# Kernel tuning notes

Hardware: AMD Instinct MI355X
Metric: run time of the kernel (lower is better)

The kernel has to match this reference:

```python
import jax, jax.numpy as jnp
from jax import lax
import numpy as np

B, T, N = 64, 512, 80
HT, HV, HI = 512, 1024, 512  # textual, visual, ilstm hidden sizes


def setup_inputs() -> dict:
    key = jax.random.key(0)
    ks = jax.random.split(key, 12)
    s = 0.02
    return {
        "h_v": jax.random.normal(ks[0], (B, T, HV), jnp.float32),
        "h_s": jax.random.normal(ks[1], (B, N, HT), jnp.float32),
        "W_S": jax.random.normal(ks[2], (HI, HT), jnp.float32) * s,
        "b_S": jnp.zeros((HI,), jnp.float32),
        "W_V": jax.random.normal(ks[3], (HI, HV), jnp.float32) * s,
        "b_V": jnp.zeros((HI,), jnp.float32),
        "W_R": jax.random.normal(ks[4], (HI, HI), jnp.float32) * s,
        "b_R": jnp.zeros((HI,), jnp.float32),
        "W_w": jax.random.normal(ks[5], (1, HI), jnp.float32) * s,
        "b_w": jnp.zeros((1,), jnp.float32),
        "W_ih": jax.random.normal(ks[6], (4 * HI, HT + HV), jnp.float32) * s,
        "b_ih": jnp.zeros((4 * HI,), jnp.float32),
        "W_hh": jax.random.normal(ks[7], (4 * HI, HI), jnp.float32) * s,
        "b_hh": jnp.zeros((4 * HI,), jnp.float32),
    }


def reference(h_v, h_s, W_S, b_S, W_V, b_V, W_R, b_R, W_w, b_w, W_ih, b_ih, W_hh, b_hh):
    n_batch, T_, _ = h_v.shape
    Hi = W_R.shape[0]
    dt = h_v.dtype
    # loop-invariant textual projection, hoisted: (B, N, Hi)
    S_proj = jnp.einsum('bnt,it->bni', h_s, W_S) + b_S
    # visual projection for all timesteps: (B, T, Hi)
    V_proj = jnp.einsum('btv,iv->bti', h_v, W_V) + b_V

    def step(carry, xs):
        h_prev, c_prev = carry
        v_t, hv_t = xs  # (B, Hi), (B, Hv)
        r_proj = h_prev @ W_R.T + b_R  # (B, Hi)
        pre = jnp.tanh(S_proj + (r_proj + v_t)[:, None, :])  # (B, N, Hi)
        beta = jnp.einsum('bni,i->bn', pre, W_w[0]) + b_w[0]  # (B, N)
        # NOTE: faithful to source -- softmax over the BATCH dim (dim=0)
        alpha = jax.nn.softmax(beta, axis=0)
        H_t_s = jnp.einsum('bnt,bn->bt', h_s, alpha)  # (B, Ht)
        r_t = jnp.concatenate([hv_t, H_t_s], axis=1)  # (B, Hv+Ht)
        gates = r_t @ W_ih.T + b_ih + h_prev @ W_hh.T + b_hh  # (B, 4Hi)
        i_g, f_g, g_g, o_g = jnp.split(gates, 4, axis=1)
        c_new = jax.nn.sigmoid(f_g) * c_prev + jax.nn.sigmoid(i_g) * jnp.tanh(g_g)
        h_new = jax.nn.sigmoid(o_g) * jnp.tanh(c_new)
        return (h_new, c_new), h_new

    init = (jnp.zeros((n_batch, Hi), dt), jnp.zeros((n_batch, Hi), dt))
    xs = (jnp.swapaxes(V_proj, 0, 1), jnp.swapaxes(h_v, 0, 1))  # time-major
    _, hs = lax.scan(step, init, xs)  # (T, B, Hi)
    return jnp.swapaxes(hs, 0, 1)  # (B, T, Hi)
```

## Files before the change

kernel.cpp:

```cpp
#include <hip/hip_runtime.h>


typedef unsigned short ushort_t;
typedef unsigned int uint_t;
typedef __attribute__((ext_vector_type(8))) short bf16x8;
typedef __attribute__((ext_vector_type(4))) float f32x4;

#define MFMA_BF16 __builtin_amdgcn_mfma_f32_16x16x32_bf16

__device__ __forceinline__ float bf2f(ushort_t u) {
  return __builtin_bit_cast(float, (uint_t)u << 16);
}
__device__ __forceinline__ ushort_t f2bf(float f) {
  uint_t u = __builtin_bit_cast(uint_t, f);
  u += 0x7FFFu + ((u >> 16) & 1u);
  return (ushort_t)(u >> 16);
}
__device__ __forceinline__ uint_t pk(float lo, float hi) {
  return (uint_t)f2bf(lo) | ((uint_t)f2bf(hi) << 16);
}
__device__ __forceinline__ void stage16(ushort_t* dst, const float* src) {
  float4 a = *(const float4*)src,     b = *(const float4*)(src + 4);
  float4 c = *(const float4*)(src + 8), d = *(const float4*)(src + 12);
  uint4 lo = { pk(a.x,a.y), pk(a.z,a.w), pk(b.x,b.y), pk(b.z,b.w) };
  uint4 hi = { pk(c.x,c.y), pk(c.z,c.w), pk(d.x,d.y), pk(d.z,d.w) };
  *(uint4*)dst = lo; *(uint4*)(dst + 8) = hi;
}
__device__ __forceinline__ bf16x8 cvt8(const float* src) {
  float4 a = *(const float4*)src, b = *(const float4*)(src + 4);
  uint4 u = { pk(a.x,a.y), pk(a.z,a.w), pk(b.x,b.y), pk(b.z,b.w) };
  return __builtin_bit_cast(bf16x8, u);
}
__device__ __forceinline__ float tanh_(float x) {
  float e = __expf(2.f * x);
  return 1.f - 2.f * __builtin_amdgcn_rcpf(e + 1.f);
}
__device__ __forceinline__ float sigm_(float x) {
  return __builtin_amdgcn_rcpf(1.f + __expf(-x));
}

__device__ __forceinline__ float ldcg_f(const float* p) {
  return __hip_atomic_load(p, __ATOMIC_RELAXED, __HIP_MEMORY_SCOPE_AGENT);
}
__device__ __forceinline__ void stcg_f(float* p, float v) {
  __hip_atomic_store(p, v, __ATOMIC_RELAXED, __HIP_MEMORY_SCOPE_AGENT);
}
__device__ __forceinline__ uint_t ldcg_u(const uint_t* p) {
  return __hip_atomic_load(p, __ATOMIC_RELAXED, __HIP_MEMORY_SCOPE_AGENT);
}
__device__ __forceinline__ void stcg_u(uint_t* p, uint_t v) {
  __hip_atomic_store(p, v, __ATOMIC_RELAXED, __HIP_MEMORY_SCOPE_AGENT);
}

__global__ __launch_bounds__(256) void cvt_kernel(
    const float* __restrict__ in, ushort_t* __restrict__ out, int n4) {
  int i = blockIdx.x * blockDim.x + threadIdx.x;
  if (i < n4) {
    float4 v = ((const float4*)in)[i];
    uint2 r = { pk(v.x, v.y), pk(v.z, v.w) };
    ((uint2*)out)[i] = r;
  }
}

__global__ __launch_bounds__(256) void pack_frag_kernel(
    const float* __restrict__ src, int ld, int coff,
    ushort_t* __restrict__ out, int mode, int lkc) {
  size_t o = ((size_t)blockIdx.x * 256 + threadIdx.x) * 8;
  int lane = (int)((o >> 3) & 63);
  int kc   = (int)((o >> 9) & ((1u << lkc) - 1u));
  int tile = (int)(o >> (9 + lkc));
  int row  = mode ? ((tile & 3) * 512 + (tile >> 2) * 16 + (lane & 15))
                  : (tile * 16 + (lane & 15));
  int col  = kc * 32 + (lane >> 4) * 8;
  const float* s = &src[(size_t)row * ld + coff + col];
  float4 a = *(const float4*)s, b = *(const float4*)(s + 4);
  uint4 u = { pk(a.x,a.y), pk(a.z,a.w), pk(b.x,b.y), pk(b.z,b.w) };
  *(uint4*)&out[o] = u;
}

__global__ __launch_bounds__(256) void gemm_bt(
    const float* __restrict__ A, int lda,
    const float* __restrict__ W, int ldw,
    const float* __restrict__ bias1,
    ushort_t* __restrict__ out, int ldo, int K, int tmaj)
{
  __shared__ __align__(16) ushort_t sA[128][32];
  __shared__ __align__(16) ushort_t sW[128][32];
  const int tid = threadIdx.x;
  const int col0 = blockIdx.x * 128, row0 = blockIdx.y * 128;
  const int lane = tid & 63, wv = tid >> 6;
  const int wr = (wv & 1) * 64, wc = (wv >> 1) * 64;
  const int fr = lane & 15, quad = lane >> 4;
  const int sr = tid >> 1, skk = (tid & 1) * 16;
  f32x4 acc[4][4] = {};
  for (int k0 = 0; k0 < K; k0 += 32) {
    stage16(&sA[sr][skk], &A[(size_t)(row0 + sr) * lda + k0 + skk]);
    stage16(&sW[sr][skk], &W[(size_t)(col0 + sr) * ldw + k0 + skk]);
    __syncthreads();
    bf16x8 af[4], wf[4];
    #pragma unroll
    for (int mt = 0; mt < 4; ++mt) af[mt] = *(const bf16x8*)&sA[wr + mt*16 + fr][quad*8];
    #pragma unroll
    for (int nt = 0; nt < 4; ++nt) wf[nt] = *(const bf16x8*)&sW[wc + nt*16 + fr][quad*8];
    #pragma unroll
    for (int mt = 0; mt < 4; ++mt)
      #pragma unroll
      for (int nt = 0; nt < 4; ++nt)
        acc[mt][nt] = MFMA_BF16(af[mt], wf[nt], acc[mt][nt], 0, 0, 0);
    __syncthreads();
  }
  #pragma unroll
  for (int nt = 0; nt < 4; ++nt) {
    int col = col0 + wc + nt*16 + fr;
    float bs = bias1 ? bias1[col] : 0.f;
    #pragma unroll
    for (int mt = 0; mt < 4; ++mt)
      #pragma unroll
      for (int r = 0; r < 4; ++r) {
        int row = row0 + wr + mt*16 + quad*4 + r;
        int orow = tmaj ? ((row & 511) * 64 + (row >> 9)) : row;
        out[(size_t)orow * ldo + col] = f2bf(acc[mt][nt][r] + bs);
      }
  }
}

__device__ __forceinline__ void spin_gen(unsigned* gen, unsigned g, unsigned* dead) {
  int n = 0;
  while (__hip_atomic_load(gen, __ATOMIC_RELAXED, __HIP_MEMORY_SCOPE_AGENT) == g) {
    __builtin_amdgcn_s_sleep(4);
    if (++n > 20000) {
      __hip_atomic_store(dead, 1u, __ATOMIC_RELAXED, __HIP_MEMORY_SCOPE_AGENT);
      break;
    }
    if ((n & 1023) == 0 &&
        __hip_atomic_load(dead, __ATOMIC_RELAXED, __HIP_MEMORY_SCOPE_AGENT) != 0u)
      break;
  }
}

__device__ __forceinline__ void grid_sync(unsigned* bar) {
  __syncthreads();
  if (threadIdx.x == 0) {
    unsigned* gen  = bar + 288;
    unsigned* dead = bar + 320;
    if (__hip_atomic_load(dead, __ATOMIC_RELAXED, __HIP_MEMORY_SCOPE_AGENT) == 0u) {
      unsigned g = __hip_atomic_load(gen, __ATOMIC_RELAXED, __HIP_MEMORY_SCOPE_AGENT);
      unsigned grp = blockIdx.x & 7u;
      unsigned old = __hip_atomic_fetch_add(bar + grp * 32, 1u,
                        __ATOMIC_RELAXED, __HIP_MEMORY_SCOPE_AGENT);
      if (old == 31u) {
        unsigned r = __hip_atomic_fetch_add(bar + 256, 1u,
                        __ATOMIC_RELAXED, __HIP_MEMORY_SCOPE_AGENT);
        if (r == 7u) {
          #pragma unroll
          for (int i = 0; i < 8; ++i)
            __hip_atomic_store(bar + i * 32, 0u, __ATOMIC_RELAXED, __HIP_MEMORY_SCOPE_AGENT);
          __hip_atomic_store(bar + 256, 0u, __ATOMIC_RELAXED, __HIP_MEMORY_SCOPE_AGENT);
          __builtin_amdgcn_s_waitcnt(0);
          __hip_atomic_store(gen, g + 1u, __ATOMIC_RELAXED, __HIP_MEMORY_SCOPE_AGENT);
        } else {
          spin_gen(gen, g, dead);
        }
      } else {
        spin_gen(gen, g, dead);
      }
    }
  }
  __syncthreads();
}

struct LoopArgs {
  const ushort_t *Sproj, *Vproj, *Xproj;
  const ushort_t *WRf, *Whhf, *Wqf, *Wihf;
  const ushort_t *hsb;
  const float *bR, *Ww, *bih, *bhh, *hv;
  float *ru, *expb, *s4;
  uint_t *hrep, *hsrep;
  unsigned *bar;
  float *out;
};


__global__ __launch_bounds__(512, 2) void loop_kernel(LoopArgs p) {
  const int blk = blockIdx.x, tid = threadIdx.x;
  const int lane = tid & 63, wv = tid >> 6;
  const int fr = lane & 15, quad = lane >> 4;
  const int b4 = (blk & 7) * 8 + (blk >> 5);
  const int q4 = (blk >> 3) & 3;

  const bool isGate = (blk < 128);
  const bool isRu   = (blk >= 128) && (blk < 144);
  const int mtG = blk >> 5;
  const int jt  = (blk & 7) * 4 + ((blk >> 3) & 3);
  const int g   = wv & 3, kh = wv >> 2;
  const int mtR = (blk - 128) >> 2;
  const int ct  = ((blk - 128) & 3) * 8 + wv;

  __shared__ __align__(16) uint_t sH[4096];
  __shared__ __align__(16) float s_ru[512];
  __shared__ __align__(16) float s_ww[512];
  __shared__ __align__(16) float s_red[512];
  __shared__ __align__(16) float s_acc[8][256];
  __shared__ float s_hsv[128];
  __shared__ float s_alpha[80];
  __shared__ float s_hh[256];
  __shared__ float s_bias[64];

  s_ww[tid] = p.Ww[tid];
  if (isGate && tid < 64) {
    int n = (tid >> 4) * 512 + jt * 16 + (tid & 15);
    s_bias[tid] = p.bih[n] + p.bhh[n];
  }
  float c_reg = 0.f;

  bf16x8 wf2[16];
  bf16x8 wfx[16];
  if (isGate) {
    #pragma unroll
    for (int kc = 0; kc < 8; ++kc) {
      int kcg = kh * 8 + kc;
      wf2[kc]     = *(const bf16x8*)&p.Whhf[((size_t)(jt*4+g)*16 + kcg)*512 + lane*8];
      wf2[8 + kc] = *(const bf16x8*)&p.Wqf [((size_t)(jt*4+g)*16 + kcg)*512 + lane*8];
    }
    if (!p.Xproj) {
      #pragma unroll
      for (int kc = 0; kc < 16; ++kc)
        wfx[kc] = *(const bf16x8*)&p.Wihf[((size_t)(jt*4+g)*32 + kh*16 + kc)*512 + lane*8];
    }
  } else if (isRu) {
    #pragma unroll
    for (int kc = 0; kc < 16; ++kc)
      wf2[kc] = *(const bf16x8*)&p.WRf[((size_t)ct*16 + kc)*512 + lane*8];
  }
  __syncthreads();

  f32x4 accA = {};
  for (int t = 0; t < 512; ++t) {
    if (isGate) {
      f32x4 acc = {};
      if (!p.Xproj) {
        int row = mtG * 16 + fr;
        #pragma unroll
        for (int kc = 0; kc < 16; ++kc) {
          bf16x8 af = cvt8(&p.hv[((size_t)row * 512 + t) * 1024 + kh*512 + kc*32 + quad*8]);
          acc = MFMA_BF16(af, wfx[kc], acc, 0, 0, 0);
        }
      }
      if (t) {
        const uint_t* src = p.hrep + mtG * 4096;
        uint_t hst[8];
        #pragma unroll
        for (int i = 0; i < 8; ++i) hst[i] = ldcg_u(src + i * 512 + tid);
        #pragma unroll
        for (int i = 0; i < 8; ++i) sH[i * 512 + tid] = hst[i];
        __syncthreads();
        #pragma unroll
        for (int kc = 0; kc < 8; ++kc) {
          int kcg = kh * 8 + kc;
          bf16x8 af = *(const bf16x8*)&sH[kcg * 256 + quad * 64 + fr * 4];
          acc = MFMA_BF16(af, wf2[kc], acc, 0, 0, 0);
        }
      }
      accA = acc;
    } else if (isRu) {
      f32x4 acc = {};
      if (t) {
        const uint_t* src = p.hrep + mtR * 4096;
        uint_t hst[8];
        #pragma unroll
        for (int i = 0; i < 8; ++i) hst[i] = ldcg_u(src + i * 512 + tid);
        #pragma unroll
        for (int i = 0; i < 8; ++i) sH[i * 512 + tid] = hst[i];
        __syncthreads();
        #pragma unroll
        for (int kc = 0; kc < 16; ++kc) {
          bf16x8 af = *(const bf16x8*)&sH[kc * 256 + quad * 64 + fr * 4];
          acc = MFMA_BF16(af, wf2[kc], acc, 0, 0, 0);
        }
      }
      #pragma unroll
      for (int r = 0; r < 4; ++r) {
        int row = mtR * 16 + quad * 4 + r, col = ct * 16 + fr;
        float v = acc[r] + p.bR[col] + bf2f(p.Vproj[(size_t)t * 32768 + row * 512 + col]);
        stcg_f(&p.ru[row * 512 + col], v);
      }
    }
    grid_sync(p.bar);

    s_ru[tid] = ldcg_f(&p.ru[b4 * 512 + tid]);
    __syncthreads();
    #pragma unroll
    for (int rr = 0; rr < 3; ++rr) {
      int nl = wv + 8 * rr;
      if (nl < 20) {
        int n = q4 * 20 + nl;
        uint4 sv = *(const uint4*)&p.Sproj[((size_t)(b4 * 80 + n)) * 512 + lane * 8];
        float4 r0 = *(const float4*)&s_ru[lane * 8];
        float4 r1 = *(const float4*)&s_ru[lane * 8 + 4];
        float4 w0 = *(const float4*)&s_ww[lane * 8];
        float4 w1 = *(const float4*)&s_ww[lane * 8 + 4];
        float a = 0.f;
        a += tanh_(bf2f((ushort_t)(sv.x & 0xFFFF)) + r0.x) * w0.x;
        a += tanh_(bf2f((ushort_t)(sv.x >> 16))    + r0.y) * w0.y;
        a += tanh_(bf2f((ushort_t)(sv.y & 0xFFFF)) + r0.z) * w0.z;
        a += tanh_(bf2f((ushort_t)(sv.y >> 16))    + r0.w) * w0.w;
        a += tanh_(bf2f((ushort_t)(sv.z & 0xFFFF)) + r1.x) * w1.x;
        a += tanh_(bf2f((ushort_t)(sv.z >> 16))    + r1.y) * w1.y;
        a += tanh_(bf2f((ushort_t)(sv.w & 0xFFFF)) + r1.z) * w1.z;
        a += tanh_(bf2f((ushort_t)(sv.w >> 16))    + r1.w) * w1.w;
        #pragma unroll
        for (int off = 32; off > 0; off >>= 1) a += __shfl_xor(a, off, 64);
        if (lane == 0) {
          float e = __expf(a);
          stcg_f(&p.expb[b4 * 80 + n], e);
          __hip_atomic_fetch_add(&p.s4[(t & 1) * 320 + (b4 & 3) * 80 + n], e,
                                 __ATOMIC_RELAXED, __HIP_MEMORY_SCOPE_AGENT);
        }
      }
    }
    grid_sync(p.bar);

    if (tid < 80) {
      const float* sc = p.s4 + (t & 1) * 320;
      float s = ldcg_f(sc + tid) + ldcg_f(sc + 80 + tid) +
                ldcg_f(sc + 160 + tid) + ldcg_f(sc + 240 + tid);
      float e = ldcg_f(&p.expb[b4 * 80 + tid]);
      s_alpha[tid] = e * __builtin_amdgcn_rcpf(s);
    }
    if (blk == 0 && tid < 320)
      stcg_f(&p.s4[((t + 1) & 1) * 320 + tid], 0.f);
    __syncthreads();
    {
      int nq = tid >> 7, jl = tid & 127;
      const ushort_t* hp = p.hsb + (size_t)b4 * 40960 + q4 * 128 + jl;
      float part = 0.f;
      #pragma unroll 5
      for (int n0 = 0; n0 < 20; ++n0) {
        int n = nq * 20 + n0;
        part += s_alpha[n] * bf2f(hp[(size_t)n * 512]);
      }
      s_red[tid] = part;
    }
    __syncthreads();
    if (tid < 128)
      s_hsv[tid] = s_red[tid] + s_red[128 + tid] + s_red[256 + tid] + s_red[384 + tid];
    __syncthreads();
    if (tid < 64) {
      int c = q4 * 128 + tid * 2;
      int kc = c >> 5, qd = (c >> 3) & 3, e2 = (c & 7) >> 1;
      int dw = (((b4 >> 4) * 16 + kc) * 4 + qd) * 64 + (b4 & 15) * 4 + e2;
      stcg_u(&p.hsrep[dw], pk(s_hsv[tid * 2], s_hsv[tid * 2 + 1]));
    }
    grid_sync(p.bar);

    if (isGate) {
      const uint_t* src = p.hsrep + mtG * 4096;
      uint_t hst[8];
      #pragma unroll
      for (int i = 0; i < 8; ++i) hst[i] = ldcg_u(src + i * 512 + tid);
      #pragma unroll
      for (int i = 0; i < 8; ++i) sH[i * 512 + tid] = hst[i];
      __syncthreads();
      f32x4 acc = accA;
      #pragma unroll
      for (int kc = 0; kc < 8; ++kc) {
        int kcg = kh * 8 + kc;
        bf16x8 af = *(const bf16x8*)&sH[kcg * 256 + quad * 64 + fr * 4];
        acc = MFMA_BF16(af, wf2[8 + kc], acc, 0, 0, 0);
      }
      #pragma unroll
      for (int r = 0; r < 4; ++r) s_acc[wv][(quad * 4 + r) * 16 + fr] = acc[r];
      __syncthreads();
      if (tid < 256) {
        int b = tid >> 4, jj = tid & 15, bi = tid;
        float g0 = s_acc[0][bi] + s_acc[4][bi] + s_bias[jj];
        float g1 = s_acc[1][bi] + s_acc[5][bi] + s_bias[16 + jj];
        float g2 = s_acc[2][bi] + s_acc[6][bi] + s_bias[32 + jj];
        float g3 = s_acc[3][bi] + s_acc[7][bi] + s_bias[48 + jj];
        if (p.Xproj) {
          const ushort_t* xp = &p.Xproj[(size_t)t * 131072 +
                                        (size_t)(mtG * 16 + b) * 2048 + jt * 16 + jj];
          g0 += bf2f(xp[0]);    g1 += bf2f(xp[512]);
          g2 += bf2f(xp[1024]); g3 += bf2f(xp[1536]);
        }
        float ig = sigm_(g0), fg = sigm_(g1), gv = tanh_(g2), og = sigm_(g3);
        float cn = fg * c_reg + ig * gv;
        c_reg = cn;
        float hn = og * tanh_(cn);
        s_hh[bi] = hn;
        p.out[((size_t)(mtG * 16 + b) * 512 + t) * 512 + jt * 16 + jj] = hn;
      }
      __syncthreads();
      if (tid < 128) {
        int b = tid >> 3, jp = tid & 7;
        int c = jt * 16 + jp * 2;
        int kc = c >> 5, qd = (c >> 3) & 3, e2 = (c & 7) >> 1;
        int dw = ((mtG * 16 + kc) * 4 + qd) * 64 + b * 4 + e2;
        stcg_u(&p.hrep[dw], pk(s_hh[b * 16 + jp * 2], s_hh[b * 16 + jp * 2 + 1]));
      }
    }
    grid_sync(p.bar);
  }
}

extern "C" void kernel_launch(void* const* d_in, const int* in_sizes, int n_in,
                              void* d_out, int out_size, void* d_ws, size_t ws_size,
                              hipStream_t stream) {
  (void)in_sizes; (void)n_in; (void)out_size;
  const float* hv   = (const float*)d_in[0];
  const float* hs   = (const float*)d_in[1];
  const float* W_S  = (const float*)d_in[2];
  const float* b_S  = (const float*)d_in[3];
  const float* W_V  = (const float*)d_in[4];
  const float* b_V  = (const float*)d_in[5];
  const float* W_R  = (const float*)d_in[6];
  const float* b_R  = (const float*)d_in[7];
  const float* W_w  = (const float*)d_in[8];
  const float* W_ih = (const float*)d_in[10];
  const float* b_ih = (const float*)d_in[11];
  const float* W_hh = (const float*)d_in[12];
  const float* b_hh = (const float*)d_in[13];

  char* ws = (char*)d_ws;
  unsigned long long off = 0;
  auto alloc = [&](unsigned long long bytes) {
    unsigned long long pp = off; off += (bytes + 255ull) & ~255ull; return pp;
  };
  ushort_t* Sproj = (ushort_t*)(ws + alloc(5120ull * 512 * 2));
  ushort_t* Vproj = (ushort_t*)(ws + alloc(512ull * 64 * 512 * 2));
  ushort_t* hsb   = (ushort_t*)(ws + alloc(64ull * 80 * 512 * 2));
  ushort_t* WRf   = (ushort_t*)(ws + alloc(512ull * 512 * 2));
  ushort_t* Whhf  = (ushort_t*)(ws + alloc(2048ull * 512 * 2));
  ushort_t* Wqf   = (ushort_t*)(ws + alloc(2048ull * 512 * 2));
  float*    ru    = (float*)(ws + alloc(64ull * 512 * 4));
  float*    expb  = (float*)(ws + alloc(64ull * 80 * 4));
  unsigned long long zoff = off;
  uint_t*   hrep  = (uint_t*)(ws + alloc(16384ull * 4));
  uint_t*   hsrep = (uint_t*)(ws + alloc(16384ull * 4));
  float*    s4    = (float*)(ws + alloc(2ull * 4 * 80 * 4));
  unsigned* bar   = (unsigned*)(ws + alloc(2048));
  unsigned long long zsize = off - zoff;
  unsigned long long tail = off;
  bool precX = ws_size >= tail + 512ull * 64 * 2048 * 2 + 4096;
  ushort_t* Xproj = precX ? (ushort_t*)(ws + tail) : nullptr;
  ushort_t* Wihf  = precX ? nullptr : (ushort_t*)(ws + tail);

  cvt_kernel<<<2560, 256, 0, stream>>>(hs, hsb, 64 * 80 * 512 / 4);
  pack_frag_kernel<<<128, 256, 0, stream>>>(W_R,  512,  0,    WRf,  0, 4);
  pack_frag_kernel<<<512, 256, 0, stream>>>(W_hh, 512,  0,    Whhf, 1, 4);
  pack_frag_kernel<<<512, 256, 0, stream>>>(W_ih, 1536, 1024, Wqf,  1, 4);
  if (!precX)
    pack_frag_kernel<<<1024, 256, 0, stream>>>(W_ih, 1536, 0, Wihf, 1, 5);

  gemm_bt<<<dim3(4, 40), 256, 0, stream>>>(hs, 512, W_S, 512, b_S, Sproj, 512, 512, 0);
  gemm_bt<<<dim3(4, 256), 256, 0, stream>>>(hv, 1024, W_V, 1024, b_V, Vproj, 512, 1024, 1);
  if (precX)
    gemm_bt<<<dim3(16, 256), 256, 0, stream>>>(hv, 1024, W_ih, 1536, nullptr, Xproj, 2048, 1024, 1);

  hipMemsetAsync(ws + zoff, 0, (size_t)zsize, stream);

  LoopArgs la;
  la.Sproj = Sproj; la.Vproj = Vproj; la.Xproj = Xproj;
  la.WRf = WRf; la.Whhf = Whhf; la.Wqf = Wqf; la.Wihf = Wihf;
  la.hsb = hsb;
  la.bR = b_R; la.Ww = W_w; la.bih = b_ih; la.bhh = b_hh; la.hv = hv;
  la.ru = ru; la.expb = expb; la.s4 = s4;
  la.hrep = hrep; la.hsrep = hsrep; la.bar = bar; la.out = (float*)d_out;
  loop_kernel<<<256, 512, 0, stream>>>(la);
}
```

Measured before the change: 12.41 ms.

## Partition persistent grid into batch groups with local barriers and counter handoff

```diff
diff --git a/kernel.cpp b/kernel.cpp
--- a/kernel.cpp
+++ b/kernel.cpp
@@ -138,24 +138,23 @@
   }
 }
 
-__device__ __forceinline__ void grid_sync(unsigned* bar) {
+__device__ __forceinline__ void sync_bar(unsigned* base, unsigned sub,
+                                         unsigned sub_last, unsigned* dead) {
   __syncthreads();
   if (threadIdx.x == 0) {
-    unsigned* gen  = bar + 288;
-    unsigned* dead = bar + 320;
+    unsigned* gen = base + 288;
     if (__hip_atomic_load(dead, __ATOMIC_RELAXED, __HIP_MEMORY_SCOPE_AGENT) == 0u) {
       unsigned g = __hip_atomic_load(gen, __ATOMIC_RELAXED, __HIP_MEMORY_SCOPE_AGENT);
-      unsigned grp = blockIdx.x & 7u;
-      unsigned old = __hip_atomic_fetch_add(bar + grp * 32, 1u,
+      unsigned old = __hip_atomic_fetch_add(base + sub * 32, 1u,
                         __ATOMIC_RELAXED, __HIP_MEMORY_SCOPE_AGENT);
-      if (old == 31u) {
-        unsigned r = __hip_atomic_fetch_add(bar + 256, 1u,
+      if (old == sub_last) {
+        unsigned r = __hip_atomic_fetch_add(base + 256, 1u,
                         __ATOMIC_RELAXED, __HIP_MEMORY_SCOPE_AGENT);
         if (r == 7u) {
           #pragma unroll
           for (int i = 0; i < 8; ++i)
-            __hip_atomic_store(bar + i * 32, 0u, __ATOMIC_RELAXED, __HIP_MEMORY_SCOPE_AGENT);
-          __hip_atomic_store(bar + 256, 0u, __ATOMIC_RELAXED, __HIP_MEMORY_SCOPE_AGENT);
+            __hip_atomic_store(base + i * 32, 0u, __ATOMIC_RELAXED, __HIP_MEMORY_SCOPE_AGENT);
+          __hip_atomic_store(base + 256, 0u, __ATOMIC_RELAXED, __HIP_MEMORY_SCOPE_AGENT);
           __builtin_amdgcn_s_waitcnt(0);
           __hip_atomic_store(gen, g + 1u, __ATOMIC_RELAXED, __HIP_MEMORY_SCOPE_AGENT);
         } else {
@@ -185,16 +184,17 @@
   const int blk = blockIdx.x, tid = threadIdx.x;
   const int lane = tid & 63, wv = tid >> 6;
   const int fr = lane & 15, quad = lane >> 4;
-  const int b4 = (blk & 7) * 8 + (blk >> 5);
-  const int q4 = (blk >> 3) & 3;
-
-  const bool isGate = (blk < 128);
-  const bool isRu   = (blk >= 128) && (blk < 144);
-  const int mtG = blk >> 5;
-  const int jt  = (blk & 7) * 4 + ((blk >> 3) & 3);
-  const int g   = wv & 3, kh = wv >> 2;
-  const int mtR = (blk - 128) >> 2;
-  const int ct  = ((blk - 128) & 3) * 8 + wv;
+  const int G = blk >> 6, w6 = blk & 63;
+  const int b4 = G * 16 + (w6 & 15), q = w6 >> 4;
+  const bool isGate = (w6 < 32);
+  const bool isRu   = (w6 >= 32) && (w6 < 36);
+  const int jt = w6 & 31;
+  const int g = wv & 3, kh = wv >> 2;
+  const int ct = ((w6 - 32) & 3) * 8 + wv;
+
+  unsigned* dead = p.bar + 320;
+  unsigned* rcnt = p.bar + 384 + G;
+  unsigned* gbar = p.bar + 512 + G * 512;
 
   __shared__ __align__(16) uint_t sH[4096];
   __shared__ __align__(16) float s_ru[512];
@@ -236,10 +236,11 @@
 
   f32x4 accA = {};
   for (int t = 0; t < 512; ++t) {
+    float x0 = 0.f, x1 = 0.f, x2 = 0.f, x3 = 0.f;
     if (isGate) {
       f32x4 acc = {};
       if (!p.Xproj) {
-        int row = mtG * 16 + fr;
+        int row = G * 16 + fr;
         #pragma unroll
         for (int kc = 0; kc < 16; ++kc) {
           bf16x8 af = cvt8(&p.hv[((size_t)row * 512 + t) * 1024 + kh*512 + kc*32 + quad*8]);
@@ -247,7 +248,7 @@
         }
       }
       if (t) {
-        const uint_t* src = p.hrep + mtG * 4096;
+        const uint_t* src = p.hrep + G * 4096;
         uint_t hst[8];
         #pragma unroll
         for (int i = 0; i < 8; ++i) hst[i] = ldcg_u(src + i * 512 + tid);
@@ -262,10 +263,16 @@
         }
       }
       accA = acc;
+      if (p.Xproj && tid < 256) {
+        const ushort_t* xp = &p.Xproj[(size_t)t * 131072 +
+                                      (size_t)(G * 16 + (tid >> 4)) * 2048 + jt * 16 + (tid & 15)];
+        x0 = bf2f(xp[0]);    x1 = bf2f(xp[512]);
+        x2 = bf2f(xp[1024]); x3 = bf2f(xp[1536]);
+      }
     } else if (isRu) {
       f32x4 acc = {};
       if (t) {
-        const uint_t* src = p.hrep + mtR * 4096;
+        const uint_t* src = p.hrep + G * 4096;
         uint_t hst[8];
         #pragma unroll
         for (int i = 0; i < 8; ++i) hst[i] = ldcg_u(src + i * 512 + tid);
@@ -280,20 +287,35 @@
       }
       #pragma unroll
       for (int r = 0; r < 4; ++r) {
-        int row = mtR * 16 + quad * 4 + r, col = ct * 16 + fr;
+        int row = G * 16 + quad * 4 + r, col = ct * 16 + fr;
         float v = acc[r] + p.bR[col] + bf2f(p.Vproj[(size_t)t * 32768 + row * 512 + col]);
         stcg_f(&p.ru[row * 512 + col], v);
       }
-    }
-    grid_sync(p.bar);
-
+      __syncthreads();
+      if (tid == 0)
+        __hip_atomic_fetch_add(rcnt, 1u, __ATOMIC_RELAXED, __HIP_MEMORY_SCOPE_AGENT);
+    }
+
+    if (tid == 0) {
+      unsigned thr = 4u * (unsigned)(t + 1);
+      int n = 0;
+      while (ldcg_u(rcnt) < thr) {
+        __builtin_amdgcn_s_sleep(4);
+        if (++n > 20000) {
+          stcg_u(dead, 1u);
+          break;
+        }
+        if ((n & 1023) == 0 && ldcg_u(dead) != 0u) break;
+      }
+    }
+    __syncthreads();
     s_ru[tid] = ldcg_f(&p.ru[b4 * 512 + tid]);
     __syncthreads();
     #pragma unroll
     for (int rr = 0; rr < 3; ++rr) {
       int nl = wv + 8 * rr;
       if (nl < 20) {
-        int n = q4 * 20 + nl;
+        int n = q * 20 + nl;
         uint4 sv = *(const uint4*)&p.Sproj[((size_t)(b4 * 80 + n)) * 512 + lane * 8];
         float4 r0 = *(const float4*)&s_ru[lane * 8];
         float4 r1 = *(const float4*)&s_ru[lane * 8 + 4];
@@ -312,27 +334,27 @@
         for (int off = 32; off > 0; off >>= 1) a += __shfl_xor(a, off, 64);
         if (lane == 0) {
           float e = __expf(a);
-          stcg_f(&p.expb[b4 * 80 + n], e);
-          __hip_atomic_fetch_add(&p.s4[(t & 1) * 320 + (b4 & 3) * 80 + n], e,
+          stcg_f(&p.expb[(t & 1) * 5120 + n * 64 + b4], e);
+          __hip_atomic_fetch_add(&p.s4[(t % 3) * 320 + G * 80 + n], e,
                                  __ATOMIC_RELAXED, __HIP_MEMORY_SCOPE_AGENT);
         }
       }
     }
-    grid_sync(p.bar);
+    sync_bar(p.bar, (unsigned)(blk & 7), 31u, dead);
 
     if (tid < 80) {
-      const float* sc = p.s4 + (t & 1) * 320;
+      const float* sc = p.s4 + (t % 3) * 320;
       float s = ldcg_f(sc + tid) + ldcg_f(sc + 80 + tid) +
                 ldcg_f(sc + 160 + tid) + ldcg_f(sc + 240 + tid);
-      float e = ldcg_f(&p.expb[b4 * 80 + tid]);
-      s_alpha[tid] = e * __builtin_amdgcn_rcpf(s);
+      float num = ldcg_f(&p.expb[(t & 1) * 5120 + tid * 64 + b4]);
+      s_alpha[tid] = num * __builtin_amdgcn_rcpf(s);
     }
     if (blk == 0 && tid < 320)
-      stcg_f(&p.s4[((t + 1) & 1) * 320 + tid], 0.f);
+      stcg_f(&p.s4[((t + 2) % 3) * 320 + tid], 0.f);
     __syncthreads();
     {
       int nq = tid >> 7, jl = tid & 127;
-      const ushort_t* hp = p.hsb + (size_t)b4 * 40960 + q4 * 128 + jl;
+      const ushort_t* hp = p.hsb + (size_t)b4 * 40960 + q * 128 + jl;
       float part = 0.f;
       #pragma unroll 5
       for (int n0 = 0; n0 < 20; ++n0) {
@@ -346,15 +368,15 @@
       s_hsv[tid] = s_red[tid] + s_red[128 + tid] + s_red[256 + tid] + s_red[384 + tid];
     __syncthreads();
     if (tid < 64) {
-      int c = q4 * 128 + tid * 2;
+      int c = q * 128 + tid * 2;
       int kc = c >> 5, qd = (c >> 3) & 3, e2 = (c & 7) >> 1;
-      int dw = (((b4 >> 4) * 16 + kc) * 4 + qd) * 64 + (b4 & 15) * 4 + e2;
+      int dw = ((G * 16 + kc) * 4 + qd) * 64 + (b4 & 15) * 4 + e2;
       stcg_u(&p.hsrep[dw], pk(s_hsv[tid * 2], s_hsv[tid * 2 + 1]));
     }
-    grid_sync(p.bar);
+    sync_bar(gbar, (unsigned)(w6 & 7), 7u, dead);
 
     if (isGate) {
-      const uint_t* src = p.hsrep + mtG * 4096;
+      const uint_t* src = p.hsrep + G * 4096;
       uint_t hst[8];
       #pragma unroll
       for (int i = 0; i < 8; ++i) hst[i] = ldcg_u(src + i * 512 + tid);
@@ -377,29 +399,24 @@
         float g1 = s_acc[1][bi] + s_acc[5][bi] + s_bias[16 + jj];
         float g2 = s_acc[2][bi] + s_acc[6][bi] + s_bias[32 + jj];
         float g3 = s_acc[3][bi] + s_acc[7][bi] + s_bias[48 + jj];
-        if (p.Xproj) {
-          const ushort_t* xp = &p.Xproj[(size_t)t * 131072 +
-                                        (size_t)(mtG * 16 + b) * 2048 + jt * 16 + jj];
-          g0 += bf2f(xp[0]);    g1 += bf2f(xp[512]);
-          g2 += bf2f(xp[1024]); g3 += bf2f(xp[1536]);
-        }
+        if (p.Xproj) { g0 += x0; g1 += x1; g2 += x2; g3 += x3; }
         float ig = sigm_(g0), fg = sigm_(g1), gv = tanh_(g2), og = sigm_(g3);
         float cn = fg * c_reg + ig * gv;
         c_reg = cn;
         float hn = og * tanh_(cn);
         s_hh[bi] = hn;
-        p.out[((size_t)(mtG * 16 + b) * 512 + t) * 512 + jt * 16 + jj] = hn;
+        p.out[((size_t)(G * 16 + b) * 512 + t) * 512 + jt * 16 + jj] = hn;
       }
       __syncthreads();
       if (tid < 128) {
         int b = tid >> 3, jp = tid & 7;
         int c = jt * 16 + jp * 2;
         int kc = c >> 5, qd = (c >> 3) & 3, e2 = (c & 7) >> 1;
-        int dw = ((mtG * 16 + kc) * 4 + qd) * 64 + b * 4 + e2;
+        int dw = ((G * 16 + kc) * 4 + qd) * 64 + b * 4 + e2;
         stcg_u(&p.hrep[dw], pk(s_hh[b * 16 + jp * 2], s_hh[b * 16 + jp * 2 + 1]));
       }
     }
-    grid_sync(p.bar);
+    sync_bar(gbar, (unsigned)(w6 & 7), 7u, dead);
   }
 }
 
@@ -433,12 +450,12 @@
   ushort_t* Whhf  = (ushort_t*)(ws + alloc(2048ull * 512 * 2));
   ushort_t* Wqf   = (ushort_t*)(ws + alloc(2048ull * 512 * 2));
   float*    ru    = (float*)(ws + alloc(64ull * 512 * 4));
-  float*    expb  = (float*)(ws + alloc(64ull * 80 * 4));
+  float*    expb  = (float*)(ws + alloc(2ull * 64 * 80 * 4));
   unsigned long long zoff = off;
   uint_t*   hrep  = (uint_t*)(ws + alloc(16384ull * 4));
   uint_t*   hsrep = (uint_t*)(ws + alloc(16384ull * 4));
-  float*    s4    = (float*)(ws + alloc(2ull * 4 * 80 * 4));
-  unsigned* bar   = (unsigned*)(ws + alloc(2048));
+  float*    s4    = (float*)(ws + alloc(3ull * 320 * 4));
+  unsigned* bar   = (unsigned*)(ws + alloc(16384));
   unsigned long long zsize = off - zoff;
   unsigned long long tail = off;
   bool precX = ws_size >= tail + 512ull * 64 * 2048 * 2 + 4096;
```

After: 11.14 ms. 10.2% less time.
